# Kernel tuning notes

Hardware: AMD Instinct MI355X
Metric: run time of the kernel (lower is better)

The kernel has to match this reference:

```python
import jax, jax.numpy as jnp
import numpy as np

B, S, H, C = 512, 16, 501, 7


def _uniform(k, shape, scale):
    return jax.random.uniform(k, shape, minval=-scale, maxval=scale, dtype=jnp.float32)


def setup_inputs() -> dict:
    key = jax.random.key(0)
    ks = jax.random.split(key, 20)
    s = 1.0 / np.sqrt(H)        # torch default init bound for Linear(H, .) and GRUCell
    se = 1.0 / np.sqrt(2 * H)   # Linear(2H, 1)
    z = jax.random.normal(ks[0], (B, H), jnp.float32)
    # strictly-lower-triangular 0/1 adjacency (DAG, ancestors have smaller index)
    dep = jax.random.randint(ks[1], (B, S, S), 0, 2).astype(jnp.float32)
    dep_graph = dep * jnp.tril(jnp.ones((S, S), jnp.float32), k=-1)
    node_encoding = jax.nn.one_hot(jax.random.randint(ks[2], (B, S), 0, C), C, dtype=jnp.float32)
    return {
        "z": z,
        "dep_graph": dep_graph,
        "node_encoding": node_encoding,
        "W_lin1": _uniform(ks[3], (H, H), s), "b_lin1": _uniform(ks[4], (H,), s),
        "W_vert": _uniform(ks[5], (C, H), s), "b_vert": _uniform(ks[6], (C,), s),
        "W_edge": _uniform(ks[7], (1, 2 * H), se), "b_edge": _uniform(ks[8], (1,), se),
        "W_gate": _uniform(ks[9], (H, H), s), "b_gate": _uniform(ks[10], (H,), s),
        "W_map": _uniform(ks[11], (H, H), s), "b_map": _uniform(ks[12], (H,), s),
        "W_ih": _uniform(ks[13], (3 * H, C), s), "b_ih": _uniform(ks[14], (3 * H,), s),
        "W_hh": _uniform(ks[15], (3 * H, H), s), "b_hh": _uniform(ks[16], (3 * H,), s),
    }


def _forward(z, dep_graph, node_encoding, W_lin1, b_lin1, W_vert, b_vert, W_edge, b_edge,
             W_gate, b_gate, W_map, b_map, W_ih, b_ih, W_hh, b_hh):
    Bs, Ss, _ = dep_graph.shape
    Hs = W_lin1.shape[0]

    def gru(x, h):  # torch.nn.GRUCell math
        gi = x @ W_ih.T + b_ih
        gh = h @ W_hh.T + b_hh
        i_r, i_z, i_n = jnp.split(gi, 3, axis=-1)
        h_r, h_z, h_n = jnp.split(gh, 3, axis=-1)
        r = jax.nn.sigmoid(i_r + h_r)
        u = jax.nn.sigmoid(i_z + h_z)
        n = jnp.tanh(i_n + r * h_n)
        return (1.0 - u) * n + u * h

    col = jnp.arange(Ss)

    def outer_step(carry, idx):
        graph_state, nhs = carry  # nhs: (B, S, H) node_hidden_state
        logits = jax.nn.softmax(graph_state @ W_vert.T + b_vert, axis=-1)  # add_vertex
        x_idx = jax.lax.dynamic_index_in_dim(node_encoding, idx, axis=1, keepdims=False)  # (B, C)
        row0 = jax.lax.dynamic_index_in_dim(dep_graph, idx, axis=1, keepdims=False)       # (B, S)

        def inner_step(ic, t):  # v_j = idx-1, ..., 0 (masked when v_j < 0)
            hv, nhs_i, row, edges = ic
            v_j = idx - 1 - t
            active = v_j >= 0
            vj = jnp.maximum(v_j, 0)
            hidden_j = jax.lax.dynamic_index_in_dim(nhs_i, vj, axis=1, keepdims=False)  # (B, H)
            p = jax.nn.sigmoid(jnp.concatenate([hv, hidden_j], axis=-1) @ W_edge.T + b_edge)  # (B,1)
            is_edge = (p[:, 0] >= 0.5).astype(z.dtype)  # hard threshold, as in source
            # emulates the in-place `ancestors[:, :v_j] = 0` on the dep_graph row
            row_new = jnp.where(col[None, :] < vj, 0.0, row)
            anc = (nhs_i * row_new[:, :, None]).reshape(-1, Hs)  # (B*S, H)
            h_in = (jax.nn.sigmoid(anc @ W_gate.T + b_gate) * (anc @ W_map.T + b_map)
                    ).reshape(Bs, Ss, Hs).sum(axis=1)  # gated-sum message aggregation
            hv_new = gru(x_idx, h_in)
            nhs_new = jax.lax.dynamic_update_index_in_dim(nhs_i, hv_new, idx, axis=1)
            edges = jnp.where(active, edges.at[:, vj].set(is_edge), edges)
            hv = jnp.where(active, hv_new, hv)
            nhs_i = jnp.where(active, nhs_new, nhs_i)
            row = jnp.where(active, row_new, row)
            return (hv, nhs_i, row, edges), None

        edges0 = jnp.zeros((Bs, Ss), z.dtype)
        (hv, nhs2, _, edges), _ = jax.lax.scan(
            inner_step, (graph_state, nhs, row0, edges0), jnp.arange(Ss - 1))
        # index == 0: no ancestors; hv = GRU(x_0, graph_state) (source leaves hv undefined here)
        hv = jnp.where(idx == 0, gru(x_idx, graph_state), hv)
        nhs3 = jax.lax.dynamic_update_index_in_dim(nhs2, hv, idx, axis=1)
        return (hv, nhs3), (logits, edges)

    graph_state0 = z @ W_lin1.T + b_lin1
    nhs0 = jnp.zeros((Bs, Ss, Hs), z.dtype)
    _, (enc, rows) = jax.lax.scan(outer_step, (graph_state0, nhs0), jnp.arange(Ss))
    gen_dep_graph = jnp.transpose(rows, (1, 0, 2))      # (B, S, S)
    gen_node_encoding = jnp.transpose(enc, (1, 0, 2))   # (B, S, C)
    return gen_dep_graph, gen_node_encoding


def reference(z, dep_graph, node_encoding, W_lin1, b_lin1, W_vert, b_vert, W_edge, b_edge,
              W_gate, b_gate, W_map, b_map, W_ih, b_ih, W_hh, b_hh):
    return _forward(z, dep_graph, node_encoding, W_lin1, b_lin1, W_vert, b_vert, W_edge,
                    b_edge, W_gate, b_gate, W_map, b_map, W_ih, b_ih, W_hh, b_hh)
```

## Files before the change

### kernel.cpp

```cpp
#include <hip/hip_runtime.h>
#include <math.h>

#define BB 512
#define SS 16
#define HH 501
#define CC 7
#define CH 128
#define PBK (4*BB)
#define OFF_ENC (BB*SS*SS)

#define BUFSZ (132*PBK)
#define O_BUFIN 0
#define O_BUFH  BUFSZ
#define O_ALIST (2*BUFSZ)
#define O_ELIST (O_ALIST + SS*BB)
#define O_CLS   (O_ELIST + SS*BB)

__device__ __forceinline__ float4 ld4(const float* p) { return *(const float4*)p; }
__device__ __forceinline__ float sigm(float x) { return 1.f / (1.f + expf(-x)); }

__device__ __forceinline__ int PACK(int k, int b) {
    return (k >> 2) * PBK + b * 4 + (k & 3);
}

__global__ __launch_bounds__(256) void k_prep(
    const float* __restrict__ z, const float* __restrict__ xenc,
    float* __restrict__ bufH, int* __restrict__ cls, float* __restrict__ out)
{
    const int b = blockIdx.x, tid = threadIdx.x;
    if (b < 256) {
        __shared__ float t[32][33];
        const int bt = b >> 4, kt = b & 15;
        const int b0 = bt * 32, k0 = kt * 32;
        const int tx = tid & 31, ty = tid >> 5;
#pragma unroll
        for (int i = 0; i < 4; ++i) {
            int row = ty + i * 8;
            t[row][tx] = (k0 + tx < HH) ? z[(b0 + row) * HH + k0 + tx] : 0.f;
        }
        __syncthreads();
#pragma unroll
        for (int i = 0; i < 4; ++i) {
            int row = ty + i * 8;
            int k = k0 + row;
            float v = (k < HH) ? t[tx][row] : 0.f;
            bufH[PACK(k, b0 + tx)] = v;
        }
    } else if (b < 264) {
        int base = (b - 256) * 1024 + tid * 4;
#pragma unroll
        for (int q = 0; q < 4; ++q) {
            int e = base + q; int s = e >> 9, bb = e & 511;
            const float* xp = xenc + (bb * SS + s) * CC;
            int c = 0;
#pragma unroll
            for (int cc = 0; cc < CC; ++cc) if (xp[cc] > 0.5f) c = cc;
            cls[s * BB + bb] = c;
        }
    } else {
        float4 z4 = make_float4(0.f, 0.f, 0.f, 0.f);
        float4* o4 = (float4*)out;
#pragma unroll
        for (int q = 0; q < 4; ++q)
            o4[(b - 264) * 1024 + q * 256 + tid] = z4;
    }
}

__global__ __launch_bounds__(256) void k_g0(
    const float* __restrict__ act, const float* __restrict__ W,
    const float* __restrict__ blin1, float* __restrict__ dst)
{
    __shared__ float wl[4][520];
    const int tid = threadIdx.x, lane = tid & 63;
    const int wv = __builtin_amdgcn_readfirstlane(tid >> 6);
    const int rg = blockIdx.x >> 2, ch = blockIdx.x & 3;
    const int r = rg * 4 + wv;
#pragma unroll
    for (int j = 0; j < 4; ++j) {
        int rr = rg * 4 + j;
        const float* src = W + (size_t)min(rr, HH - 1) * HH;
        bool ok = rr < HH;
        for (int k = tid; k < 512; k += 256)
            wl[j][k] = (ok && k < HH) ? src[k] : 0.f;
    }
    __syncthreads();
    const int c0 = ch * 128 + lane, c1 = c0 + 64;
    const float* a0 = act + c0 * 4;
    const float* a1 = act + c1 * 4;
    float4 A0[4], A1[4], Wb[2];
#pragma unroll
    for (int q = 0; q < 3; ++q) { A0[q] = ld4(a0 + q * PBK); A1[q] = ld4(a1 + q * PBK); }
    Wb[0] = ld4(&wl[wv][0]);
    float s0 = 0.f, s1 = 0.f;
#pragma unroll 4
    for (int kc = 0; kc < CH; ++kc) {
        int kn = kc + 3;
        A0[kn & 3] = ld4(a0 + (size_t)kn * PBK);
        A1[kn & 3] = ld4(a1 + (size_t)kn * PBK);
        int kw = min(kc + 1, CH - 1);
        Wb[(kc + 1) & 1] = ld4(&wl[wv][kw * 4]);
        float4 w = Wb[kc & 1], x0 = A0[kc & 3], x1 = A1[kc & 3];
        s0 = fmaf(w.x, x0.x, s0); s0 = fmaf(w.y, x0.y, s0);
        s0 = fmaf(w.z, x0.z, s0); s0 = fmaf(w.w, x0.w, s0);
        s1 = fmaf(w.x, x1.x, s1); s1 = fmaf(w.y, x1.y, s1);
        s1 = fmaf(w.z, x1.z, s1); s1 = fmaf(w.w, x1.w, s1);
    }
    if (r < HH) {
        float bv = blin1[r];
        dst[PACK(r, c0)] = s0 + bv;
        dst[PACK(r, c1)] = s1 + bv;
    }
}

__global__ __launch_bounds__(256) void k_gru(
    const float* __restrict__ act, const float* __restrict__ Whh,
    const int* __restrict__ cls,
    const float* __restrict__ bhh, const float* __restrict__ Wih,
    const float* __restrict__ bih, int idx, float* __restrict__ dst)
{
    __shared__ float wl[12][520];
    const int tid = threadIdx.x, lane = tid & 63;
    const int wv = __builtin_amdgcn_readfirstlane(tid >> 6);
    const int rg = blockIdx.x >> 2, ch = blockIdx.x & 3;
    const int r = rg * 4 + wv;
#pragma unroll
    for (int j = 0; j < 12; ++j) {
        int g = j >> 2, rl = j & 3, rr = rg * 4 + rl;
        const float* src = Whh + (size_t)(g * HH + min(rr, HH - 1)) * HH;
        bool ok = rr < HH;
        for (int k = tid; k < 512; k += 256)
            wl[j][k] = (ok && k < HH) ? src[k] : 0.f;
    }
    const int c0 = ch * 128 + lane, c1 = c0 + 64;
    const int cc0 = cls[idx * BB + c0], cc1 = cls[idx * BB + c1];
    const float hp0 = act[PACK(min(r, HH - 1), c0)];
    const float hp1 = act[PACK(min(r, HH - 1), c1)];
    __syncthreads();
    const float* a0 = act + c0 * 4;
    const float* a1 = act + c1 * 4;
    float4 A0[4], A1[4], Wb[2][3];
#pragma unroll
    for (int q = 0; q < 3; ++q) { A0[q] = ld4(a0 + q * PBK); A1[q] = ld4(a1 + q * PBK); }
#pragma unroll
    for (int g = 0; g < 3; ++g) Wb[0][g] = ld4(&wl[g * 4 + wv][0]);
    float acc[6] = {};
#pragma unroll 4
    for (int kc = 0; kc < CH; ++kc) {
        int kn = kc + 3;
        A0[kn & 3] = ld4(a0 + (size_t)kn * PBK);
        A1[kn & 3] = ld4(a1 + (size_t)kn * PBK);
        int kw = min(kc + 1, CH - 1);
#pragma unroll
        for (int g = 0; g < 3; ++g) Wb[(kc + 1) & 1][g] = ld4(&wl[g * 4 + wv][kw * 4]);
        float4 x0 = A0[kc & 3], x1 = A1[kc & 3];
#pragma unroll
        for (int g = 0; g < 3; ++g) {
            float4 w = Wb[kc & 1][g];
            acc[g*2+0] = fmaf(w.x, x0.x, acc[g*2+0]); acc[g*2+0] = fmaf(w.y, x0.y, acc[g*2+0]);
            acc[g*2+0] = fmaf(w.z, x0.z, acc[g*2+0]); acc[g*2+0] = fmaf(w.w, x0.w, acc[g*2+0]);
            acc[g*2+1] = fmaf(w.x, x1.x, acc[g*2+1]); acc[g*2+1] = fmaf(w.y, x1.y, acc[g*2+1]);
            acc[g*2+1] = fmaf(w.z, x1.z, acc[g*2+1]); acc[g*2+1] = fmaf(w.w, x1.w, acc[g*2+1]);
        }
    }
    if (r < HH) {
        float bi0 = bih[r], bi1 = bih[HH + r], bi2 = bih[2 * HH + r];
        float bh0 = bhh[r], bh1 = bhh[HH + r], bh2 = bhh[2 * HH + r];
        float w0c0 = Wih[(0 * HH + r) * CC + cc0], w1c0 = Wih[(1 * HH + r) * CC + cc0],
              w2c0 = Wih[(2 * HH + r) * CC + cc0];
        float w0c1 = Wih[(0 * HH + r) * CC + cc1], w1c1 = Wih[(1 * HH + r) * CC + cc1],
              w2c1 = Wih[(2 * HH + r) * CC + cc1];
        {
            float rgt = sigm(w0c0 + bi0 + acc[0] + bh0);
            float ugt = sigm(w1c0 + bi1 + acc[2] + bh1);
            float ngt = tanhf(w2c0 + bi2 + rgt * (acc[4] + bh2));
            dst[PACK(r, c0)] = (1.f - ugt) * ngt + ugt * hp0;
        }
        {
            float rgt = sigm(w0c1 + bi0 + acc[1] + bh0);
            float ugt = sigm(w1c1 + bi1 + acc[3] + bh1);
            float ngt = tanhf(w2c1 + bi2 + rgt * (acc[5] + bh2));
            dst[PACK(r, c1)] = (1.f - ugt) * ngt + ugt * hp1;
        }
    }
}

__global__ __launch_bounds__(256) void k_post(
    const float* __restrict__ actH, const float* __restrict__ actIn,
    const float* __restrict__ Wgate, const float* __restrict__ bgate,
    const float* __restrict__ Wmap,  const float* __restrict__ bmap,
    const float* __restrict__ dep,
    const float* __restrict__ Wedge, const float* __restrict__ bedge,
    const float* __restrict__ Wvert, const float* __restrict__ bvert,
    int idx, int ngemm, int dsrc,
    float* __restrict__ dst, float* __restrict__ Alist,
    float* __restrict__ Elist, float* __restrict__ out)
{
    __shared__ float wl[9][520];
    const int tid = threadIdx.x, lane = tid & 63;
    const int wv = __builtin_amdgcn_readfirstlane(tid >> 6);
    if ((int)blockIdx.x < ngemm) {
        const int rg = blockIdx.x >> 2, ch = blockIdx.x & 3;
        const int r = rg * 4 + wv;
#pragma unroll
        for (int j = 0; j < 8; ++j) {
            int t2 = j >> 2, rl = j & 3, rr = rg * 4 + rl;
            const float* src = (t2 ? Wmap : Wgate) + (size_t)min(rr, HH - 1) * HH;
            bool ok = rr < HH;
            for (int k = tid; k < 512; k += 256)
                wl[j][k] = (ok && k < HH) ? src[k] : 0.f;
        }
        const int c0 = ch * 128 + lane, c1 = c0 + 64;
        const float d0 = dep[c0 * (SS * SS) + (idx + 1) * SS + idx];
        const float d1 = dep[c1 * (SS * SS) + (idx + 1) * SS + idx];
        __syncthreads();
        const float* a0 = actH + c0 * 4;
        const float* a1 = actH + c1 * 4;
        float4 A0[4], A1[4], Wb[2][2];
#pragma unroll
        for (int q = 0; q < 3; ++q) { A0[q] = ld4(a0 + q * PBK); A1[q] = ld4(a1 + q * PBK); }
#pragma unroll
        for (int t2 = 0; t2 < 2; ++t2) Wb[0][t2] = ld4(&wl[t2 * 4 + wv][0]);
        float acc[4] = {};
#pragma unroll 4
        for (int kc = 0; kc < CH; ++kc) {
            int kn = kc + 3;
            A0[kn & 3] = ld4(a0 + (size_t)kn * PBK);
            A1[kn & 3] = ld4(a1 + (size_t)kn * PBK);
            int kw = min(kc + 1, CH - 1);
#pragma unroll
            for (int t2 = 0; t2 < 2; ++t2) Wb[(kc + 1) & 1][t2] = ld4(&wl[t2 * 4 + wv][kw * 4]);
            float4 x0 = A0[kc & 3], x1 = A1[kc & 3];
#pragma unroll
            for (int t2 = 0; t2 < 2; ++t2) {
                float4 w = Wb[kc & 1][t2];
                acc[t2*2+0] = fmaf(w.x, x0.x, acc[t2*2+0]); acc[t2*2+0] = fmaf(w.y, x0.y, acc[t2*2+0]);
                acc[t2*2+0] = fmaf(w.z, x0.z, acc[t2*2+0]); acc[t2*2+0] = fmaf(w.w, x0.w, acc[t2*2+0]);
                acc[t2*2+1] = fmaf(w.x, x1.x, acc[t2*2+1]); acc[t2*2+1] = fmaf(w.y, x1.y, acc[t2*2+1]);
                acc[t2*2+1] = fmaf(w.z, x1.z, acc[t2*2+1]); acc[t2*2+1] = fmaf(w.w, x1.w, acc[t2*2+1]);
            }
        }
        if (r < HH) {
            float bgv = bgate[r], bmv = bmap[r];
            float c0v = sigm(bgv) * bmv;
            float f0 = sigm(acc[0] + bgv) * (acc[2] + bmv);
            float f1 = sigm(acc[1] + bgv) * (acc[3] + bmv);
            dst[PACK(r, c0)] = (d0 != 0.f) ? (f0 + 15.f * c0v) : (16.f * c0v);
            dst[PACK(r, c1)] = (d1 != 0.f) ? (f1 + 15.f * c0v) : (16.f * c0v);
        }
    } else {
#pragma unroll
        for (int j = 0; j < 9; ++j) {
            const float* src = (j < 2) ? (Wedge + j * HH) : (Wvert + (j - 2) * HH);
            for (int k = tid; k < 512; k += 256)
                wl[j][k] = (k < HH) ? src[k] : 0.f;
        }
        __syncthreads();
        const int db = ((int)blockIdx.x - ngemm) * 256 + tid;
        const float* hp = (dsrc ? actH : actIn) + db * 4;
        float4 Ab[4];
#pragma unroll
        for (int q = 0; q < 3; ++q) Ab[q] = ld4(hp + q * PBK);
        float p[9];
#pragma unroll
        for (int j = 0; j < 9; ++j) p[j] = 0.f;
#pragma unroll 4
        for (int kc = 0; kc < CH; ++kc) {
            int kn = kc + 3;
            Ab[kn & 3] = ld4(hp + (size_t)kn * PBK);
            float4 x = Ab[kc & 3];
#pragma unroll
            for (int j = 0; j < 9; ++j) {
                float4 w = ld4(&wl[j][kc * 4]);
                p[j] = fmaf(w.x, x.x, p[j]); p[j] = fmaf(w.y, x.y, p[j]);
                p[j] = fmaf(w.z, x.z, p[j]); p[j] = fmaf(w.w, x.w, p[j]);
            }
        }
        if (idx >= 0) { Alist[idx * BB + db] = p[0]; Elist[idx * BB + db] = p[1]; }
        if (idx <= SS - 2) {
            float lv[CC]; float mx = -1e30f;
#pragma unroll
            for (int c = 0; c < CC; ++c) { lv[c] = p[2 + c] + bvert[c]; mx = fmaxf(mx, lv[c]); }
            float sum = 0.f; float ev[CC];
#pragma unroll
            for (int c = 0; c < CC; ++c) { ev[c] = expf(lv[c] - mx); sum += ev[c]; }
            float inv = 1.f / sum;
#pragma unroll
            for (int c = 0; c < CC; ++c)
                out[OFF_ENC + (db * SS + (idx + 1)) * CC + c] = ev[c] * inv;
        }
        if (idx >= 1) {
            float be = bedge[0];
            float aprev = Alist[(idx - 1) * BB + db], eprev = Elist[(idx - 1) * BB + db];
            out[db * SS * SS + idx * SS + (idx - 1)] =
                (aprev + eprev + be >= 0.f) ? 1.f : 0.f;
            for (int vj = 0; vj <= idx - 2; ++vj)
                out[db * SS * SS + idx * SS + vj] =
                    (p[0] + Elist[vj * BB + db] + be >= 0.f) ? 1.f : 0.f;
        }
    }
}

extern "C" void kernel_launch(void* const* d_in, const int* in_sizes, int n_in,
                              void* d_out, int out_size, void* d_ws, size_t ws_size,
                              hipStream_t stream)
{
    const float* z     = (const float*)d_in[0];
    const float* dep   = (const float*)d_in[1];
    const float* xenc  = (const float*)d_in[2];
    const float* Wlin1 = (const float*)d_in[3];
    const float* blin1 = (const float*)d_in[4];
    const float* Wvert = (const float*)d_in[5];
    const float* bvert = (const float*)d_in[6];
    const float* Wedge = (const float*)d_in[7];
    const float* bedge = (const float*)d_in[8];
    const float* Wgate = (const float*)d_in[9];
    const float* bgate = (const float*)d_in[10];
    const float* Wmap  = (const float*)d_in[11];
    const float* bmap  = (const float*)d_in[12];
    const float* Wih   = (const float*)d_in[13];
    const float* bih   = (const float*)d_in[14];
    const float* Whh   = (const float*)d_in[15];
    const float* bhh   = (const float*)d_in[16];
    float* out = (float*)d_out;

    float* ws    = (float*)d_ws;
    float* bufIn = ws + O_BUFIN;
    float* bufH  = ws + O_BUFH;
    float* Alist = ws + O_ALIST;
    float* Elist = ws + O_ELIST;
    int*   cls   = (int*)(ws + O_CLS);

    k_prep<<<296, 256, 0, stream>>>(z, xenc, bufH, cls, out);
    k_g0<<<504, 256, 0, stream>>>(bufH, Wlin1, blin1, bufIn);
    k_post<<<2, 256, 0, stream>>>(bufH, bufIn, Wgate, bgate, Wmap, bmap, dep,
                                  Wedge, bedge, Wvert, bvert, -1, 0, 0,
                                  bufIn, Alist, Elist, out);
    for (int idx = 0; idx < SS; ++idx) {
        k_gru<<<504, 256, 0, stream>>>(bufIn, Whh, cls, bhh, Wih, bih, idx, bufH);
        int ng = (idx < SS - 1) ? 504 : 0;
        k_post<<<ng + 2, 256, 0, stream>>>(bufH, bufIn, Wgate, bgate, Wmap, bmap,
                                           dep, Wedge, bedge, Wvert, bvert,
                                           idx, ng, 1,
                                           bufIn, Alist, Elist, out);
    }
}
```

Baseline: 1.312 ms.

## Halve batch columns per thread, swizzle block mapping, deepen activation prefetch

Each GEMV-style block now handles 64 batch columns instead of 128, doubling the grid to 1024 blocks. A decode swizzle groups 8 row-groups with 8 column chunks so neighbouring blocks share weight rows and activation columns in cache. The activation prefetch ring grows from 4 to 8 float4 entries, the buffer is padded so those prefetches stay in bounds, and launch bounds request 4 blocks per CU. The aim is more occupancy and latency hiding, at the cost of loading each weight row into LDS twice as often and running some early-exit padding blocks.

```diff
diff --git a/kernel.cpp b/kernel.cpp
--- a/kernel.cpp
+++ b/kernel.cpp
@@ -9,7 +9,7 @@
 #define PBK (4*BB)
 #define OFF_ENC (BB*SS*SS)
 
-#define BUFSZ (132*PBK)
+#define BUFSZ (136*PBK)
 #define O_BUFIN 0
 #define O_BUFH  BUFSZ
 #define O_ALIST (2*BUFSZ)
@@ -21,6 +21,12 @@
 
 __device__ __forceinline__ int PACK(int k, int b) {
     return (k >> 2) * PBK + b * 4 + (k & 3);
+}
+
+__device__ __forceinline__ bool decode(int bidx, int& rg, int& ch) {
+    rg = (bidx & 7) | ((bidx >> 6) << 3);
+    ch = (bidx >> 3) & 7;
+    return rg < 126;
 }
 
 __global__ __launch_bounds__(256) void k_prep(
@@ -66,14 +72,15 @@
     }
 }
 
-__global__ __launch_bounds__(256) void k_g0(
+__global__ __launch_bounds__(256, 4) void k_g0(
     const float* __restrict__ act, const float* __restrict__ W,
     const float* __restrict__ blin1, float* __restrict__ dst)
 {
-    __shared__ float wl[4][520];
+    int rg, ch;
+    if (!decode(blockIdx.x, rg, ch)) return;
+    __shared__ float wl[4][512];
     const int tid = threadIdx.x, lane = tid & 63;
     const int wv = __builtin_amdgcn_readfirstlane(tid >> 6);
-    const int rg = blockIdx.x >> 2, ch = blockIdx.x & 3;
     const int r = rg * 4 + wv;
 #pragma unroll
     for (int j = 0; j < 4; ++j) {
@@ -84,44 +91,41 @@
             wl[j][k] = (ok && k < HH) ? src[k] : 0.f;
     }
     __syncthreads();
-    const int c0 = ch * 128 + lane, c1 = c0 + 64;
-    const float* a0 = act + c0 * 4;
-    const float* a1 = act + c1 * 4;
-    float4 A0[4], A1[4], Wb[2];
-#pragma unroll
-    for (int q = 0; q < 3; ++q) { A0[q] = ld4(a0 + q * PBK); A1[q] = ld4(a1 + q * PBK); }
-    Wb[0] = ld4(&wl[wv][0]);
-    float s0 = 0.f, s1 = 0.f;
-#pragma unroll 4
-    for (int kc = 0; kc < CH; ++kc) {
-        int kn = kc + 3;
-        A0[kn & 3] = ld4(a0 + (size_t)kn * PBK);
-        A1[kn & 3] = ld4(a1 + (size_t)kn * PBK);
-        int kw = min(kc + 1, CH - 1);
-        Wb[(kc + 1) & 1] = ld4(&wl[wv][kw * 4]);
-        float4 w = Wb[kc & 1], x0 = A0[kc & 3], x1 = A1[kc & 3];
-        s0 = fmaf(w.x, x0.x, s0); s0 = fmaf(w.y, x0.y, s0);
-        s0 = fmaf(w.z, x0.z, s0); s0 = fmaf(w.w, x0.w, s0);
-        s1 = fmaf(w.x, x1.x, s1); s1 = fmaf(w.y, x1.y, s1);
-        s1 = fmaf(w.z, x1.z, s1); s1 = fmaf(w.w, x1.w, s1);
-    }
-    if (r < HH) {
-        float bv = blin1[r];
-        dst[PACK(r, c0)] = s0 + bv;
-        dst[PACK(r, c1)] = s1 + bv;
-    }
-}
-
-__global__ __launch_bounds__(256) void k_gru(
+    const int c = ch * 64 + lane;
+    const float* ap = act + c * 4;
+    float4 A[8];
+#pragma unroll
+    for (int q = 0; q < 8; ++q) A[q] = ld4(ap + q * PBK);
+    float4 Wr[2];
+    Wr[0] = ld4(&wl[wv][0]);
+    float acc = 0.f;
+    for (int t = 0; t < 16; ++t) {
+#pragma unroll
+        for (int u = 0; u < 8; ++u) {
+            const int kc = t * 8 + u;
+            float4 x = A[u];
+            A[u] = ld4(ap + (kc + 8) * PBK);
+            float4 w = Wr[kc & 1];
+            int kw = (kc + 1 < CH) ? kc + 1 : CH - 1;
+            Wr[(kc + 1) & 1] = ld4(&wl[wv][kw * 4]);
+            acc = fmaf(w.x, x.x, acc); acc = fmaf(w.y, x.y, acc);
+            acc = fmaf(w.z, x.z, acc); acc = fmaf(w.w, x.w, acc);
+        }
+    }
+    if (r < HH) dst[PACK(r, c)] = acc + blin1[r];
+}
+
+__global__ __launch_bounds__(256, 4) void k_gru(
     const float* __restrict__ act, const float* __restrict__ Whh,
     const int* __restrict__ cls,
     const float* __restrict__ bhh, const float* __restrict__ Wih,
     const float* __restrict__ bih, int idx, float* __restrict__ dst)
 {
-    __shared__ float wl[12][520];
+    int rg, ch;
+    if (!decode(blockIdx.x, rg, ch)) return;
+    __shared__ float wl[12][512];
     const int tid = threadIdx.x, lane = tid & 63;
     const int wv = __builtin_amdgcn_readfirstlane(tid >> 6);
-    const int rg = blockIdx.x >> 2, ch = blockIdx.x & 3;
     const int r = rg * 4 + wv;
 #pragma unroll
     for (int j = 0; j < 12; ++j) {
@@ -131,60 +135,50 @@
         for (int k = tid; k < 512; k += 256)
             wl[j][k] = (ok && k < HH) ? src[k] : 0.f;
     }
-    const int c0 = ch * 128 + lane, c1 = c0 + 64;
-    const int cc0 = cls[idx * BB + c0], cc1 = cls[idx * BB + c1];
-    const float hp0 = act[PACK(min(r, HH - 1), c0)];
-    const float hp1 = act[PACK(min(r, HH - 1), c1)];
+    const int c = ch * 64 + lane;
+    const int cc = cls[idx * BB + c];
+    const float hp = act[PACK(min(r, HH - 1), c)];
     __syncthreads();
-    const float* a0 = act + c0 * 4;
-    const float* a1 = act + c1 * 4;
-    float4 A0[4], A1[4], Wb[2][3];
-#pragma unroll
-    for (int q = 0; q < 3; ++q) { A0[q] = ld4(a0 + q * PBK); A1[q] = ld4(a1 + q * PBK); }
-#pragma unroll
-    for (int g = 0; g < 3; ++g) Wb[0][g] = ld4(&wl[g * 4 + wv][0]);
-    float acc[6] = {};
-#pragma unroll 4
-    for (int kc = 0; kc < CH; ++kc) {
-        int kn = kc + 3;
-        A0[kn & 3] = ld4(a0 + (size_t)kn * PBK);
-        A1[kn & 3] = ld4(a1 + (size_t)kn * PBK);
-        int kw = min(kc + 1, CH - 1);
-#pragma unroll
-        for (int g = 0; g < 3; ++g) Wb[(kc + 1) & 1][g] = ld4(&wl[g * 4 + wv][kw * 4]);
-        float4 x0 = A0[kc & 3], x1 = A1[kc & 3];
-#pragma unroll
-        for (int g = 0; g < 3; ++g) {
-            float4 w = Wb[kc & 1][g];
-            acc[g*2+0] = fmaf(w.x, x0.x, acc[g*2+0]); acc[g*2+0] = fmaf(w.y, x0.y, acc[g*2+0]);
-            acc[g*2+0] = fmaf(w.z, x0.z, acc[g*2+0]); acc[g*2+0] = fmaf(w.w, x0.w, acc[g*2+0]);
-            acc[g*2+1] = fmaf(w.x, x1.x, acc[g*2+1]); acc[g*2+1] = fmaf(w.y, x1.y, acc[g*2+1]);
-            acc[g*2+1] = fmaf(w.z, x1.z, acc[g*2+1]); acc[g*2+1] = fmaf(w.w, x1.w, acc[g*2+1]);
+    const float* ap = act + c * 4;
+    float4 A[8];
+#pragma unroll
+    for (int q = 0; q < 8; ++q) A[q] = ld4(ap + q * PBK);
+    float4 W0[2], W1[2], W2[2];
+    W0[0] = ld4(&wl[0 * 4 + wv][0]);
+    W1[0] = ld4(&wl[1 * 4 + wv][0]);
+    W2[0] = ld4(&wl[2 * 4 + wv][0]);
+    float a0 = 0.f, a1 = 0.f, a2 = 0.f;
+    for (int t = 0; t < 16; ++t) {
+#pragma unroll
+        for (int u = 0; u < 8; ++u) {
+            const int kc = t * 8 + u;
+            float4 x = A[u];
+            A[u] = ld4(ap + (kc + 8) * PBK);
+            float4 w0 = W0[kc & 1], w1 = W1[kc & 1], w2 = W2[kc & 1];
+            int kw = (kc + 1 < CH) ? kc + 1 : CH - 1;
+            W0[(kc + 1) & 1] = ld4(&wl[0 * 4 + wv][kw * 4]);
+            W1[(kc + 1) & 1] = ld4(&wl[1 * 4 + wv][kw * 4]);
+            W2[(kc + 1) & 1] = ld4(&wl[2 * 4 + wv][kw * 4]);
+            a0 = fmaf(w0.x, x.x, a0); a0 = fmaf(w0.y, x.y, a0);
+            a0 = fmaf(w0.z, x.z, a0); a0 = fmaf(w0.w, x.w, a0);
+            a1 = fmaf(w1.x, x.x, a1); a1 = fmaf(w1.y, x.y, a1);
+            a1 = fmaf(w1.z, x.z, a1); a1 = fmaf(w1.w, x.w, a1);
+            a2 = fmaf(w2.x, x.x, a2); a2 = fmaf(w2.y, x.y, a2);
+            a2 = fmaf(w2.z, x.z, a2); a2 = fmaf(w2.w, x.w, a2);
         }
     }
     if (r < HH) {
-        float bi0 = bih[r], bi1 = bih[HH + r], bi2 = bih[2 * HH + r];
-        float bh0 = bhh[r], bh1 = bhh[HH + r], bh2 = bhh[2 * HH + r];
-        float w0c0 = Wih[(0 * HH + r) * CC + cc0], w1c0 = Wih[(1 * HH + r) * CC + cc0],
-              w2c0 = Wih[(2 * HH + r) * CC + cc0];
-        float w0c1 = Wih[(0 * HH + r) * CC + cc1], w1c1 = Wih[(1 * HH + r) * CC + cc1],
-              w2c1 = Wih[(2 * HH + r) * CC + cc1];
-        {
-            float rgt = sigm(w0c0 + bi0 + acc[0] + bh0);
-            float ugt = sigm(w1c0 + bi1 + acc[2] + bh1);
-            float ngt = tanhf(w2c0 + bi2 + rgt * (acc[4] + bh2));
-            dst[PACK(r, c0)] = (1.f - ugt) * ngt + ugt * hp0;
-        }
-        {
-            float rgt = sigm(w0c1 + bi0 + acc[1] + bh0);
-            float ugt = sigm(w1c1 + bi1 + acc[3] + bh1);
-            float ngt = tanhf(w2c1 + bi2 + rgt * (acc[5] + bh2));
-            dst[PACK(r, c1)] = (1.f - ugt) * ngt + ugt * hp1;
-        }
-    }
-}
-
-__global__ __launch_bounds__(256) void k_post(
+        float gi0 = Wih[(0 * HH + r) * CC + cc] + bih[r];
+        float gi1 = Wih[(1 * HH + r) * CC + cc] + bih[HH + r];
+        float gi2 = Wih[(2 * HH + r) * CC + cc] + bih[2 * HH + r];
+        float rgt = sigm(gi0 + a0 + bhh[r]);
+        float ugt = sigm(gi1 + a1 + bhh[HH + r]);
+        float ngt = tanhf(gi2 + rgt * (a2 + bhh[2 * HH + r]));
+        dst[PACK(r, c)] = (1.f - ugt) * ngt + ugt * hp;
+    }
+}
+
+__global__ __launch_bounds__(256, 4) void k_post(
     const float* __restrict__ actH, const float* __restrict__ actIn,
     const float* __restrict__ Wgate, const float* __restrict__ bgate,
     const float* __restrict__ Wmap,  const float* __restrict__ bmap,
@@ -195,11 +189,12 @@
     float* __restrict__ dst, float* __restrict__ Alist,
     float* __restrict__ Elist, float* __restrict__ out)
 {
-    __shared__ float wl[9][520];
+    __shared__ float wl[9][512];
     const int tid = threadIdx.x, lane = tid & 63;
     const int wv = __builtin_amdgcn_readfirstlane(tid >> 6);
     if ((int)blockIdx.x < ngemm) {
-        const int rg = blockIdx.x >> 2, ch = blockIdx.x & 3;
+        int rg, ch;
+        if (!decode(blockIdx.x, rg, ch)) return;
         const int r = rg * 4 + wv;
 #pragma unroll
         for (int j = 0; j < 8; ++j) {
@@ -209,43 +204,38 @@
             for (int k = tid; k < 512; k += 256)
                 wl[j][k] = (ok && k < HH) ? src[k] : 0.f;
         }
-        const int c0 = ch * 128 + lane, c1 = c0 + 64;
-        const float d0 = dep[c0 * (SS * SS) + (idx + 1) * SS + idx];
-        const float d1 = dep[c1 * (SS * SS) + (idx + 1) * SS + idx];
+        const int c = ch * 64 + lane;
+        const float d = dep[c * (SS * SS) + (idx + 1) * SS + idx];
         __syncthreads();
-        const float* a0 = actH + c0 * 4;
-        const float* a1 = actH + c1 * 4;
-        float4 A0[4], A1[4], Wb[2][2];
-#pragma unroll
-        for (int q = 0; q < 3; ++q) { A0[q] = ld4(a0 + q * PBK); A1[q] = ld4(a1 + q * PBK); }
-#pragma unroll
-        for (int t2 = 0; t2 < 2; ++t2) Wb[0][t2] = ld4(&wl[t2 * 4 + wv][0]);
-        float acc[4] = {};
-#pragma unroll 4
-        for (int kc = 0; kc < CH; ++kc) {
-            int kn = kc + 3;
-            A0[kn & 3] = ld4(a0 + (size_t)kn * PBK);
-            A1[kn & 3] = ld4(a1 + (size_t)kn * PBK);
-            int kw = min(kc + 1, CH - 1);
-#pragma unroll
-            for (int t2 = 0; t2 < 2; ++t2) Wb[(kc + 1) & 1][t2] = ld4(&wl[t2 * 4 + wv][kw * 4]);
-            float4 x0 = A0[kc & 3], x1 = A1[kc & 3];
-#pragma unroll
-            for (int t2 = 0; t2 < 2; ++t2) {
-                float4 w = Wb[kc & 1][t2];
-                acc[t2*2+0] = fmaf(w.x, x0.x, acc[t2*2+0]); acc[t2*2+0] = fmaf(w.y, x0.y, acc[t2*2+0]);
-                acc[t2*2+0] = fmaf(w.z, x0.z, acc[t2*2+0]); acc[t2*2+0] = fmaf(w.w, x0.w, acc[t2*2+0]);
-                acc[t2*2+1] = fmaf(w.x, x1.x, acc[t2*2+1]); acc[t2*2+1] = fmaf(w.y, x1.y, acc[t2*2+1]);
-                acc[t2*2+1] = fmaf(w.z, x1.z, acc[t2*2+1]); acc[t2*2+1] = fmaf(w.w, x1.w, acc[t2*2+1]);
+        const float* ap = actH + c * 4;
+        float4 A[8];
+#pragma unroll
+        for (int q = 0; q < 8; ++q) A[q] = ld4(ap + q * PBK);
+        float4 W0[2], W1[2];
+        W0[0] = ld4(&wl[0 * 4 + wv][0]);
+        W1[0] = ld4(&wl[1 * 4 + wv][0]);
+        float a0 = 0.f, a1 = 0.f;
+        for (int t = 0; t < 16; ++t) {
+#pragma unroll
+            for (int u = 0; u < 8; ++u) {
+                const int kc = t * 8 + u;
+                float4 x = A[u];
+                A[u] = ld4(ap + (kc + 8) * PBK);
+                float4 w0 = W0[kc & 1], w1 = W1[kc & 1];
+                int kw = (kc + 1 < CH) ? kc + 1 : CH - 1;
+                W0[(kc + 1) & 1] = ld4(&wl[0 * 4 + wv][kw * 4]);
+                W1[(kc + 1) & 1] = ld4(&wl[1 * 4 + wv][kw * 4]);
+                a0 = fmaf(w0.x, x.x, a0); a0 = fmaf(w0.y, x.y, a0);
+                a0 = fmaf(w0.z, x.z, a0); a0 = fmaf(w0.w, x.w, a0);
+                a1 = fmaf(w1.x, x.x, a1); a1 = fmaf(w1.y, x.y, a1);
+                a1 = fmaf(w1.z, x.z, a1); a1 = fmaf(w1.w, x.w, a1);
             }
         }
         if (r < HH) {
             float bgv = bgate[r], bmv = bmap[r];
             float c0v = sigm(bgv) * bmv;
-            float f0 = sigm(acc[0] + bgv) * (acc[2] + bmv);
-            float f1 = sigm(acc[1] + bgv) * (acc[3] + bmv);
-            dst[PACK(r, c0)] = (d0 != 0.f) ? (f0 + 15.f * c0v) : (16.f * c0v);
-            dst[PACK(r, c1)] = (d1 != 0.f) ? (f1 + 15.f * c0v) : (16.f * c0v);
+            float f = sigm(a0 + bgv) * (a1 + bmv);
+            dst[PACK(r, c)] = (d != 0.f) ? (f + 15.f * c0v) : (16.f * c0v);
         }
     } else {
 #pragma unroll
@@ -257,22 +247,24 @@
         __syncthreads();
         const int db = ((int)blockIdx.x - ngemm) * 256 + tid;
         const float* hp = (dsrc ? actH : actIn) + db * 4;
-        float4 Ab[4];
-#pragma unroll
-        for (int q = 0; q < 3; ++q) Ab[q] = ld4(hp + q * PBK);
+        float4 A[8];
+#pragma unroll
+        for (int q = 0; q < 8; ++q) A[q] = ld4(hp + q * PBK);
         float p[9];
 #pragma unroll
         for (int j = 0; j < 9; ++j) p[j] = 0.f;
-#pragma unroll 4
-        for (int kc = 0; kc < CH; ++kc) {
-            int kn = kc + 3;
-            Ab[kn & 3] = ld4(hp + (size_t)kn * PBK);
-            float4 x = Ab[kc & 3];
-#pragma unroll
-            for (int j = 0; j < 9; ++j) {
-                float4 w = ld4(&wl[j][kc * 4]);
-                p[j] = fmaf(w.x, x.x, p[j]); p[j] = fmaf(w.y, x.y, p[j]);
-                p[j] = fmaf(w.z, x.z, p[j]); p[j] = fmaf(w.w, x.w, p[j]);
+        for (int t = 0; t < 16; ++t) {
+#pragma unroll
+            for (int u = 0; u < 8; ++u) {
+                const int kc = t * 8 + u;
+                float4 x = A[u];
+                A[u] = ld4(hp + (kc + 8) * PBK);
+#pragma unroll
+                for (int j = 0; j < 9; ++j) {
+                    float4 w = ld4(&wl[j][kc * 4]);
+                    p[j] = fmaf(w.x, x.x, p[j]); p[j] = fmaf(w.y, x.y, p[j]);
+                    p[j] = fmaf(w.z, x.z, p[j]); p[j] = fmaf(w.w, x.w, p[j]);
+                }
             }
         }
         if (idx >= 0) { Alist[idx * BB + db] = p[0]; Elist[idx * BB + db] = p[1]; }
@@ -331,13 +323,13 @@
     int*   cls   = (int*)(ws + O_CLS);
 
     k_prep<<<296, 256, 0, stream>>>(z, xenc, bufH, cls, out);
-    k_g0<<<504, 256, 0, stream>>>(bufH, Wlin1, blin1, bufIn);
+    k_g0<<<1024, 256, 0, stream>>>(bufH, Wlin1, blin1, bufIn);
     k_post<<<2, 256, 0, stream>>>(bufH, bufIn, Wgate, bgate, Wmap, bmap, dep,
                                   Wedge, bedge, Wvert, bvert, -1, 0, 0,
                                   bufIn, Alist, Elist, out);
     for (int idx = 0; idx < SS; ++idx) {
-        k_gru<<<504, 256, 0, stream>>>(bufIn, Whh, cls, bhh, Wih, bih, idx, bufH);
-        int ng = (idx < SS - 1) ? 504 : 0;
+        k_gru<<<1024, 256, 0, stream>>>(bufIn, Whh, cls, bhh, Wih, bih, idx, bufH);
+        int ng = (idx < SS - 1) ? 1024 : 0;
         k_post<<<ng + 2, 256, 0, stream>>>(bufH, bufIn, Wgate, bgate, Wmap, bmap,
                                            dep, Wedge, bedge, Wvert, bvert,
                                            idx, ng, 1,
```

Measured after the change: 1.563 ms. 1.19x slower.
